# Kernel optimization log

Hardware: AMD Instinct MI355X
Metric: run time of the kernel (lower is better)

Reference implementation:

```python
import jax, jax.numpy as jnp
import numpy as np

R1, R2 = 0.1, 0.2  # initial_radius(0.0125) * 8, * 16
EPS = 1e-5

def sqdist(a, b):
    # a [B,N,3], b [B,M,3] -> [B,N,M]
    return jnp.sum(a * a, -1)[:, :, None] + jnp.sum(b * b, -1)[:, None, :] - 2.0 * jnp.einsum('bnc,bmc->bnm', a, b)

def gather(p, idx):
    # p [B,N,C], idx [B,...] -> [B,...,C]
    return jax.vmap(lambda pp, ii: pp[ii])(p, idx)

def fps(xyz, npoint):
    # farthest point sampling, returns int32 [B,npoint]
    B, N, _ = xyz.shape
    def step(carry, _):
        dist, far = carry
        cen = xyz[jnp.arange(B), far]                       # [B,3]
        d = jnp.sum((xyz - cen[:, None, :]) ** 2, -1)       # [B,N]
        dist = jnp.minimum(dist, d)
        nxt = jnp.argmax(dist, -1).astype(jnp.int32)
        return (dist, nxt), far
    init = (jnp.full((B, N), 1e10, xyz.dtype), jnp.zeros(B, jnp.int32))
    _, idx = jax.lax.scan(step, init, None, length=npoint)
    return idx.T

def ball_query(xyz, new_xyz, radius, nsample):
    d = sqdist(new_xyz, xyz)                                # [B,S,N]
    N = xyz.shape[1]
    cand = jnp.where(d <= radius * radius, jnp.arange(N, dtype=jnp.int32), jnp.int32(N))
    idx = -jax.lax.top_k(-cand, nsample)[0]                 # smallest nsample in-ball indices
    first = idx[..., :1]
    idx = jnp.where(idx == N, first, idx)                   # pad with first neighbor
    nearest = jnp.argmin(d, -1, keepdims=True).astype(jnp.int32)
    return jnp.where(idx == N, nearest, idx)                # fallback if ball empty

def bn_relu(x, g, b, axes):
    # training-mode batchnorm (biased var) + relu, channel-last
    m = jnp.mean(x, axes, keepdims=True)
    v = jnp.mean((x - m) ** 2, axes, keepdims=True)
    return jax.nn.relu((x - m) * jax.lax.rsqrt(v + EPS) * g + b)

def set_abstraction(xyz, feat, npoint, radius, nsample, layers):
    new_xyz = gather(xyz, fps(xyz, npoint))                 # [B,S,3]
    gidx = ball_query(xyz, new_xyz, radius, nsample)        # [B,S,K]
    gx = gather(xyz, gidx) - new_xyz[:, :, None, :]         # [B,S,K,3]
    h = jnp.concatenate([gx, gather(feat, gidx)], -1)       # [B,S,K,3+C]
    for w, g, b in layers:
        h = bn_relu(jnp.einsum('bskc,oc->bsko', h, w), g, b, (0, 1, 2))
    return new_xyz, jnp.max(h, 2)                           # [B,S,Cout]

def set_upconv(pos1, pos2, feat1, feat2, nsample, w1, g1, b1, w2, g2, b2):
    idx = jax.lax.top_k(-sqdist(pos1, pos2), nsample)[1]    # knn into sparse cloud [B,N,K]
    gp = gather(pos2, idx) - pos1[:, :, None, :]
    h = jnp.concatenate([gather(feat2, idx), gp], -1)       # [B,N,K,C2+3]
    h = bn_relu(jnp.einsum('bnkc,oc->bnko', h, w1), g1, b1, (0, 1, 2))
    h = jnp.max(h, 2)
    h = jnp.concatenate([h, feat1], -1)                     # [B,N,mlp[-1]+C1]
    return bn_relu(jnp.einsum('bnc,oc->bno', h, w2), g2, b2, (0, 1))

def feature_prop(pos1, pos2, feat1, feat2, w, g, b):
    negd, idx = jax.lax.top_k(-sqdist(pos1, pos2), 3)       # 3-NN
    dist = jnp.maximum(-negd, 1e-10)
    wgt = 1.0 / dist
    wgt = wgt / jnp.sum(wgt, -1, keepdims=True)
    interp = jnp.sum(gather(feat2, idx) * wgt[..., None], 2)
    h = jnp.concatenate([interp, feat1], -1)
    return bn_relu(jnp.einsum('bnc,oc->bno', h, w), g, b, (0, 1))

def _forward(points1, fea1, points2, fea2,
             sa1_w0, sa1_g0, sa1_b0, sa1_w1, sa1_g1, sa1_b1,
             sa2_w0, sa2_g0, sa2_b0, sa2_w1, sa2_g1, sa2_b1,
             su1_w1, su1_g1, su1_b1, su1_w2, su1_g2, su1_b2,
             fp_w, fp_g, fp_b, bn1_g, bn1_b, conv2_w, conv2_b):
    def pipeline(pts, fea):
        l1x, l1f = set_abstraction(pts, fea, 4096, R1, 16,
                                   [(sa1_w0, sa1_g0, sa1_b0), (sa1_w1, sa1_g1, sa1_b1)])
        l2x, l2f = set_abstraction(l1x, l1f, 1024, R2, 16,
                                   [(sa2_w0, sa2_g0, sa2_b0), (sa2_w1, sa2_g1, sa2_b1)])
        l1n = set_upconv(l1x, l2x, l1f, l2f, 8, su1_w1, su1_g1, su1_b1, su1_w2, su1_g2, su1_b2)
        l0n = feature_prop(pts, l1x, fea, l1n, fp_w, fp_g, fp_b)
        x = bn_relu(l0n, bn1_g, bn1_b, (0, 1))              # relu(bn1(.))
        sf = jnp.einsum('bnc,oc->bno', x, conv2_w) + conv2_b
        return jnp.concatenate([pts, sf], -1)               # include_pos
    return jnp.stack([pipeline(points1, fea1), pipeline(points2, fea2)])  # [2,B,N,19]

def setup_inputs() -> dict:
    key = jax.random.key(0)
    ks = jax.random.split(key, 12)
    B, N, C = 2, 8192, 10
    def w(k, o, i):
        return jax.random.normal(k, (o, i), jnp.float32) * 0.1
    inp = {
        'points1': jax.random.uniform(ks[0], (B, N, 3), jnp.float32),
        'fea1': jax.random.normal(ks[1], (B, N, C), jnp.float32),
        'points2': jax.random.uniform(ks[2], (B, N, 3), jnp.float32),
        'fea2': jax.random.normal(ks[3], (B, N, C), jnp.float32),
        'sa1_w0': w(ks[4], 16, 13), 'sa1_g0': jnp.ones(16), 'sa1_b0': jnp.zeros(16),
        'sa1_w1': w(ks[5], 32, 16), 'sa1_g1': jnp.ones(32), 'sa1_b1': jnp.zeros(32),
        'sa2_w0': w(ks[6], 32, 35), 'sa2_g0': jnp.ones(32), 'sa2_b0': jnp.zeros(32),
        'sa2_w1': w(ks[7], 64, 32), 'sa2_g1': jnp.ones(64), 'sa2_b1': jnp.zeros(64),
        'su1_w1': w(ks[8], 32, 67), 'su1_g1': jnp.ones(32), 'su1_b1': jnp.zeros(32),
        'su1_w2': w(ks[9], 32, 64), 'su1_g2': jnp.ones(32), 'su1_b2': jnp.zeros(32),
        'fp_w': w(ks[10], 32, 42), 'fp_g': jnp.ones(32), 'fp_b': jnp.zeros(32),
        'bn1_g': jnp.ones(32), 'bn1_b': jnp.zeros(32),
        'conv2_w': w(ks[11], 16, 32), 'conv2_b': jnp.zeros(16),
    }
    return inp

def reference(points1, fea1, points2, fea2,
              sa1_w0, sa1_g0, sa1_b0, sa1_w1, sa1_g1, sa1_b1,
              sa2_w0, sa2_g0, sa2_b0, sa2_w1, sa2_g1, sa2_b1,
              su1_w1, su1_g1, su1_b1, su1_w2, su1_g2, su1_b2,
              fp_w, fp_g, fp_b, bn1_g, bn1_b, conv2_w, conv2_b):
    return _forward(points1, fea1, points2, fea2,
                    sa1_w0, sa1_g0, sa1_b0, sa1_w1, sa1_g1, sa1_b1,
                    sa2_w0, sa2_g0, sa2_b0, sa2_w1, sa2_g1, sa2_b1,
                    su1_w1, su1_g1, su1_b1, su1_w2, su1_g2, su1_b2,
                    fp_w, fp_g, fp_b, bn1_g, bn1_b, conv2_w, conv2_b)
```

## Files before the change

### kernel.cpp

```cpp
#include <hip/hip_runtime.h>

#define DI __device__ __forceinline__

enum : int {
  OFF_XYZF = 0,
  OFF_FEAF = OFF_XYZF + 4*8192*3,
  OFF_NX1  = OFF_FEAF + 4*8192*10,
  OFF_L1F  = OFF_NX1  + 4*4096*3,
  OFF_NX2  = OFF_L1F  + 4*4096*32,
  OFF_L2F  = OFF_NX2  + 4*1024*3,
  OFF_UH2  = OFF_L2F  + 4*1024*64,
  OFF_L1N  = OFF_UH2  + 4*4096*32,
  OFF_H3   = OFF_L1N  + 4*4096*32,
  OFF_L0N  = OFF_H3   + 4*8192*32,
  OFF_STATS= OFF_L0N  + 4*8192*32,
  OFF_GIDX1= OFF_STATS + 2048,
  OFF_GIDX2= OFF_GIDX1 + 4*4096*16,
  OFF_UIDX = OFF_GIDX2 + 4*1024*16,
  WS_END   = OFF_UIDX + 4*4096*8
};
enum : int { ST_SA1A=0, ST_SA1B=64, ST_SA2A=128, ST_SA2B=192, ST_U1=320, ST_U2=384, ST_FP=448, ST_BN1=512 };

DI float nrm3(float x, float y, float z){ return fmaf(z,z, fmaf(y,y, x*x)); }
DI float dot3(float ax,float ay,float az,float bx,float by,float bz){
  return fmaf(az,bz, fmaf(ay,by, ax*bx));
}

template<int CTRL>
DI float dppmax_f(float v){
  int o = __builtin_amdgcn_update_dpp(0, __float_as_int(v), CTRL, 0xf, 0xf, true);
  return fmaxf(v, __int_as_float(o));
}
template<int CTRL>
DI int dppmin_i(int v){
  int o = __builtin_amdgcn_update_dpp(0x7fffffff, v, CTRL, 0xf, 0xf, false);
  return v < o ? v : o;
}
DI float red63_fmax(float v){
  v = dppmax_f<0x111>(v);
  v = dppmax_f<0x112>(v);
  v = dppmax_f<0x114>(v);
  v = dppmax_f<0x118>(v);
  v = dppmax_f<0x142>(v);
  v = dppmax_f<0x143>(v);
  return v;
}
DI int red63_imin(int v){
  v = dppmin_i<0x111>(v);
  v = dppmin_i<0x112>(v);
  v = dppmin_i<0x114>(v);
  v = dppmin_i<0x118>(v);
  v = dppmin_i<0x142>(v);
  v = dppmin_i<0x143>(v);
  return v;
}

template<int CH>
DI void stats_accum(float* h, float* dst, float (*sred)[128])
{
  float sq[CH];
  #pragma unroll
  for (int c=0;c<CH;c++) sq[c]=h[c]*h[c];
  #pragma unroll
  for (int m=1;m<64;m<<=1){
    #pragma unroll
    for (int c=0;c<CH;c++){ h[c] += __shfl_xor(h[c], m, 64); sq[c] += __shfl_xor(sq[c], m, 64); }
  }
  const int tid=threadIdx.x, wid=tid>>6, lane=tid&63;
  if (lane==0){
    #pragma unroll
    for (int c=0;c<CH;c++){ sred[wid][c]=h[c]; sred[wid][CH+c]=sq[c]; }
  }
  __syncthreads();
  if (tid < 2*CH){
    float v = sred[0][tid]+sred[1][tid]+sred[2][tid]+sred[3][tid];
    atomicAdd(dst+tid, v);
  }
}

__global__ __launch_bounds__(256) void prep(const float* __restrict__ p1,const float* __restrict__ f1,
                                            const float* __restrict__ p2,const float* __restrict__ f2,
                                            float* __restrict__ xyzf, float* __restrict__ feaf)
{
  const int i = blockIdx.x*256+threadIdx.x;
  const int z = i>>13, n = i&8191, pipe=z>>1, b=z&1;
  const float* ps = (pipe?p2:p1) + (b*8192+n)*3;
  const float* fs = (pipe?f2:f1) + (b*8192+n)*10;
  float* xo = xyzf + (z*8192+n)*3;
  float* fo = feaf + (z*8192+n)*10;
  #pragma unroll
  for (int c=0;c<3;c++)  xo[c]=ps[c];
  #pragma unroll
  for (int c=0;c<10;c++) fo[c]=fs[c];
}

DI int mspread(int v){ return (v&1) | ((v&2)<<2) | ((v&4)<<4); }

template<int N,int NPOINT>
__global__ __launch_bounds__(512) void fps_lane(const float* __restrict__ src, float* __restrict__ dst)
{
  constexpr int T=512, P=N/T;
  const int z = blockIdx.x;
  const float* xyz = src + z*N*3;
  float* nx = dst + z*NPOINT*3;
  const int t = threadIdx.x, w = t>>6, lane = t&63;

  __shared__ float sx[N], sy[N], szz[N];
  __shared__ int hist[512], offs[512], wsum[8];
  __shared__ int sidx[N];
  __shared__ unsigned long long s_wk[2][8];

  hist[t]=0;
  __syncthreads();
  int code_[P];
  #pragma unroll
  for (int i=0;i<P;i++){
    const int j = t + i*T;
    float x=xyz[j*3], y=xyz[j*3+1], zz=xyz[j*3+2];
    sx[j]=x; sy[j]=y; szz[j]=zz;
    int a=(int)(x*8.f);  a=a<0?0:(a>7?7:a);
    int b=(int)(y*8.f);  b=b<0?0:(b>7?7:b);
    int c=(int)(zz*8.f); c=c<0?0:(c>7?7:c);
    int mc = mspread(a) | (mspread(b)<<1) | (mspread(c)<<2);
    code_[i]=mc;
    atomicAdd(&hist[mc],1);
  }
  __syncthreads();
  {
    int x = hist[t];
    int ix = x;
    #pragma unroll
    for (int m=1;m<64;m<<=1){ int y=__shfl_up(ix,m,64); if (lane>=m) ix+=y; }
    if (lane==63) wsum[w]=ix;
    __syncthreads();
    int base=0;
    #pragma unroll
    for (int q=0;q<7;q++) base += (q<w)? wsum[q] : 0;
    offs[t] = base + ix - x;
  }
  __syncthreads();
  #pragma unroll
  for (int i=0;i<P;i++){
    int pos = atomicAdd(&offs[code_[i]],1);
    sidx[pos] = t + i*T;
  }
  __syncthreads();
  float px[P],py[P],pz[P],dist[P]; int oi[P];
  #pragma unroll
  for (int k=0;k<P;k++){
    const int j = sidx[t*P+k];
    oi[k]=j;
    px[k]=sx[j]; py[k]=sy[j]; pz[k]=szz[j];
    dist[k]=1e10f;
  }
  float blox=px[0],bhix=px[0],bloy=py[0],bhiy=py[0],bloz=pz[0],bhiz=pz[0];
  int jb = oi[0];
  #pragma unroll
  for (int k=1;k<P;k++){
    blox=fminf(blox,px[k]); bhix=fmaxf(bhix,px[k]);
    bloy=fminf(bloy,py[k]); bhiy=fmaxf(bhiy,py[k]);
    bloz=fminf(bloz,pz[k]); bhiz=fmaxf(bhiz,pz[k]);
    jb = oi[k]<jb ? oi[k] : jb;
  }
  float lm = 1e10f;

  for (int s=0;;s++){
    float wmv = red63_fmax(lm);
    float swm = __int_as_float(__builtin_amdgcn_readlane(__float_as_int(wmv), 63));
    int jc = (lm==swm) ? jb : 0x7fffffff;
    int jcv = red63_imin(jc);
    int sjw = __builtin_amdgcn_readlane(jcv, 63);
    if (lane==0)
      s_wk[s&1][w] = ((unsigned long long)__float_as_uint(swm)<<32)
                   | (unsigned)(N-1-sjw);
    __syncthreads();
    unsigned long long bk = s_wk[s&1][0];
    #pragma unroll
    for (int q=1;q<8;q++){ unsigned long long o=s_wk[s&1][q]; bk = o>bk?o:bk; }
    const int cur = (N-1) - (int)(unsigned)(bk & 0xffffffffull);
    if (t==0){ nx[s*3]=sx[cur]; nx[s*3+1]=sy[cur]; nx[s*3+2]=szz[cur]; }
    if (s==NPOINT-1) break;
    const float cx=sx[cur], cy=sy[cur], cz=szz[cur];
    float dxm = fmaxf(fmaxf(blox-cx, cx-bhix), 0.f);
    float dym = fmaxf(fmaxf(bloy-cy, cy-bhiy), 0.f);
    float dzm = fmaxf(fmaxf(bloz-cz, cz-bhiz), 0.f);
    float lb  = fmaf(dzm,dzm, fmaf(dym,dym, dxm*dxm));
    if (lb*0.99999f < lm){
      float a=-1.f, b2=-1.f;
      #pragma unroll
      for (int k=0;k<P;k+=2){
        float dx0=px[k]-cx,   dy0=py[k]-cy,   dz0=pz[k]-cz;
        float dx1=px[k+1]-cx, dy1=py[k+1]-cy, dz1=pz[k+1]-cz;
        float d0 = fmaf(dz0,dz0, fmaf(dy0,dy0, dx0*dx0));
        float d1 = fmaf(dz1,dz1, fmaf(dy1,dy1, dx1*dx1));
        float n0 = fminf(dist[k],   d0);
        float n1 = fminf(dist[k+1], d1);
        dist[k]=n0; dist[k+1]=n1;
        a=fmaxf(a,n0); b2=fmaxf(b2,n1);
      }
      lm = fmaxf(a,b2);
      int nj = 0x7fffffff;
      #pragma unroll
      for (int k=0;k<P;k++){
        int cand = (dist[k]==lm) ? oi[k] : 0x7fffffff;
        nj = cand<nj ? cand : nj;
      }
      jb = nj;
    }
  }
}

template<int NSRC,int SQ,int K>
__global__ __launch_bounds__(64) void ball_query(const float* __restrict__ qxyz, const float* __restrict__ sxyz,
                                                 int* __restrict__ gidx, float r2)
{
  __shared__ float4 tile[1024];
  const int z = blockIdx.y, tid = threadIdx.x;
  const int s = blockIdx.x*64 + tid;
  const float* q = qxyz + (z*SQ+s)*3;
  const float qx=q[0],qy=q[1],qz=q[2];
  const float qq=nrm3(qx,qy,qz);
  int cnt=0, first=0, amin=0; float dmin=3.0e38f;
  int* out = gidx + (z*SQ+s)*K;
  for (int t0=0;t0<NSRC;t0+=1024){
    __syncthreads();
    for (int i=tid;i<1024;i+=64){
      const float* p = sxyz + (z*NSRC+t0+i)*3;
      float x=p[0],y=p[1],w=p[2];
      tile[i]=make_float4(x,y,w,nrm3(x,y,w));
    }
    __syncthreads();
    for (int jj=0;jj<1024;jj++){
      float4 p = tile[jj];
      float dot=dot3(qx,qy,qz,p.x,p.y,p.z);
      float d=(qq+p.w)-2.0f*dot;
      const int j = t0+jj;
      if (d < dmin){ dmin=d; amin=j; }
      if (d <= r2 && cnt < K){ if(cnt==0) first=j; out[cnt]=j; cnt++; }
    }
  }
  const int fill = (cnt==0)? amin : first;
  for (int c=cnt;c<K;c++) out[c]=fill;
}

template<int S,int K,int CF,int C1,int C2,int NSRC,int PASS>
__global__ __launch_bounds__(256) void sa_pass(
    const float* __restrict__ srcxyz, const float* __restrict__ srcfea,
    const float* __restrict__ qxyz, const int* __restrict__ gidx,
    const float* __restrict__ w0, const float* __restrict__ g0, const float* __restrict__ b0,
    const float* __restrict__ w1, const float* __restrict__ g1v, const float* __restrict__ b1v,
    float* __restrict__ stats, int offA, int offB, float cnt0, float cnt1,
    float* __restrict__ outp)
{
  constexpr int CIN = 3+CF;
  __shared__ float w0l[C1*CIN];
  __shared__ float w1l[PASS>=2 ? C2*C1 : 1];
  __shared__ float sc0[C1], bi0[C1];
  __shared__ float sc1[C2], bi1[C2];
  __shared__ float sred[4][128];
  const int z = blockIdx.y, pipe = z>>1, tid = threadIdx.x;
  float* stA = stats + pipe*1024 + offA;
  float* stB = stats + pipe*1024 + offB;
  for (int i=tid;i<C1*CIN;i+=256) w0l[i]=w0[i];
  if (PASS>=2){
    for (int i=tid;i<C2*C1;i+=256) w1l[i]=w1[i];
    if (tid<C1){
      float m = stA[tid]/cnt0;
      float var = stA[C1+tid]/cnt0 - m*m;
      float rs = 1.0f/sqrtf(var+1e-5f);
      float sc = rs*g0[tid];
      sc0[tid]=sc; bi0[tid]=b0[tid]-m*sc;
    }
  }
  if (PASS==3 && tid<C2){
    float m = stB[tid]/cnt1;
    float var = stB[C2+tid]/cnt1 - m*m;
    float rs = 1.0f/sqrtf(var+1e-5f);
    float sc = rs*g1v[tid];
    sc1[tid]=sc; bi1[tid]=b1v[tid]-m*sc;
  }
  __syncthreads();
  const int item = blockIdx.x*256+tid;
  const int s = item/K;
  const int j = gidx[(z*S+s)*K + (item%K)];
  const float* q = qxyz + (z*S+s)*3;
  const float* p = srcxyz + (z*NSRC+j)*3;
  float f[CIN];
  f[0]=p[0]-q[0]; f[1]=p[1]-q[1]; f[2]=p[2]-q[2];
  const float* fe = srcfea + (z*NSRC+j)*CF;
  #pragma unroll
  for (int c=0;c<CF;c++) f[3+c]=fe[c];
  float h1[C1];
  #pragma unroll
  for (int o=0;o<C1;o++){
    float a=0.f;
    #pragma unroll
    for (int c=0;c<CIN;c++) a = fmaf(w0l[o*CIN+c], f[c], a);
    h1[o]=a;
  }
  if (PASS==1){ stats_accum<C1>(h1, stA, sred); return; }
  float f2v[C1];
  #pragma unroll
  for (int o=0;o<C1;o++) f2v[o]=fmaxf(fmaf(h1[o],sc0[o],bi0[o]), 0.f);
  float h2[C2];
  #pragma unroll
  for (int o=0;o<C2;o++){
    float a=0.f;
    #pragma unroll
    for (int c=0;c<C1;c++) a = fmaf(w1l[o*C1+c], f2v[c], a);
    h2[o]=a;
  }
  if (PASS==2){ stats_accum<C2>(h2, stB, sred); return; }
  #pragma unroll
  for (int o=0;o<C2;o++) h2[o]=fmaxf(fmaf(h2[o],sc1[o],bi1[o]), 0.f);
  #pragma unroll
  for (int msk=1; msk<K; msk<<=1){
    #pragma unroll
    for (int o=0;o<C2;o++) h2[o]=fmaxf(h2[o], __shfl_xor(h2[o], msk, 64));
  }
  if ((tid & (K-1))==0){
    float* op = outp + (z*S+s)*C2;
    #pragma unroll
    for (int o=0;o<C2;o++) op[o]=h2[o];
  }
}

__global__ __launch_bounds__(64) void up_top8(const float* __restrict__ nx1, const float* __restrict__ nx2,
                                              int* __restrict__ uidx)
{
  __shared__ float4 tile[1024];
  const int z=blockIdx.y, tid=threadIdx.x;
  const int s=blockIdx.x*64+tid;
  const float* q = nx1 + (z*4096+s)*3;
  const float qx=q[0],qy=q[1],qz=q[2];
  const float qq=nrm3(qx,qy,qz);
  for (int i=tid;i<1024;i+=64){
    const float* p = nx2 + (z*1024+i)*3;
    float x=p[0],y=p[1],w=p[2];
    tile[i]=make_float4(x,y,w,nrm3(x,y,w));
  }
  __syncthreads();
  float d[8]; int id[8];
  #pragma unroll
  for (int r=0;r<8;r++){ d[r]=3e38f; id[r]=0; }
  for (int j=0;j<1024;j++){
    float4 p=tile[j];
    float dt=dot3(qx,qy,qz,p.x,p.y,p.z);
    float dd=(qq+p.w)-2.0f*dt;
    if (dd<d[7]){
      d[7]=dd; id[7]=j;
      #pragma unroll
      for (int r=7;r>0;r--){
        if (d[r]<d[r-1]){ float td=d[r-1]; d[r-1]=d[r]; d[r]=td; int ti=id[r-1]; id[r-1]=id[r]; id[r]=ti; }
      }
    }
  }
  int* o = uidx + (z*4096+s)*8;
  #pragma unroll
  for (int r=0;r<8;r++) o[r]=id[r];
}

template<int PASS>
__global__ __launch_bounds__(256) void up_pass(
    const float* __restrict__ nx1, const float* __restrict__ nx2,
    const float* __restrict__ l2f, const float* __restrict__ l1f,
    const int* __restrict__ uidx,
    const float* __restrict__ w1, const float* __restrict__ g1v, const float* __restrict__ b1v,
    const float* __restrict__ w2,
    float* __restrict__ stats, float* __restrict__ uh2)
{
  __shared__ float w1l[32*67];
  __shared__ float w2l[PASS==2?32*64:1];
  __shared__ float sc0[32], bi0[32];
  __shared__ float sred[4][128];
  const int z=blockIdx.y, pipe=z>>1, tid=threadIdx.x;
  float* stU1 = stats + pipe*1024 + ST_U1;
  float* stU2 = stats + pipe*1024 + ST_U2;
  for (int i=tid;i<32*67;i+=256) w1l[i]=w1[i];
  if (PASS==2){
    for (int i=tid;i<32*64;i+=256) w2l[i]=w2[i];
    if (tid<32){
      float m=stU1[tid]/65536.f;
      float var=stU1[32+tid]/65536.f - m*m;
      float rs=1.0f/sqrtf(var+1e-5f);
      float sc=rs*g1v[tid];
      sc0[tid]=sc; bi0[tid]=b1v[tid]-m*sc;
    }
  }
  __syncthreads();
  const int item = blockIdx.x*256+tid;
  const int s = item>>3, k = item&7;
  const int j = uidx[(z*4096+s)*8+k];
  float f67[67];
  const float* fe = l2f + (z*1024+j)*64;
  #pragma unroll
  for (int c=0;c<64;c++) f67[c]=fe[c];
  const float* pp = nx2 + (z*1024+j)*3;
  const float* qv = nx1 + (z*4096+s)*3;
  f67[64]=pp[0]-qv[0]; f67[65]=pp[1]-qv[1]; f67[66]=pp[2]-qv[2];
  float h[32];
  #pragma unroll
  for (int o=0;o<32;o++){
    float a=0.f;
    #pragma unroll
    for (int c=0;c<67;c++) a=fmaf(w1l[o*67+c], f67[c], a);
    h[o]=a;
  }
  if (PASS==1){ stats_accum<32>(h, stU1, sred); return; }
  #pragma unroll
  for (int o=0;o<32;o++) h[o]=fmaxf(fmaf(h[o],sc0[o],bi0[o]),0.f);
  #pragma unroll
  for (int msk=1; msk<8; msk<<=1){
    #pragma unroll
    for (int o=0;o<32;o++) h[o]=fmaxf(h[o], __shfl_xor(h[o],msk,64));
  }
  float h2[32];
  if (k==0){
    const float* l1 = l1f + (z*4096+s)*32;
    #pragma unroll
    for (int o=0;o<32;o++){
      float a=0.f;
      #pragma unroll
      for (int c=0;c<32;c++) a=fmaf(w2l[o*64+c], h[c], a);
      #pragma unroll
      for (int c=0;c<32;c++) a=fmaf(w2l[o*64+32+c], l1[c], a);
      h2[o]=a;
    }
    float* up = uh2 + (z*4096+s)*32;
    #pragma unroll
    for (int o=0;o<32;o++) up[o]=h2[o];
  } else {
    #pragma unroll
    for (int o=0;o<32;o++) h2[o]=0.f;
  }
  stats_accum<32>(h2, stU2, sred);
}

__global__ __launch_bounds__(256) void up_norm(const float* __restrict__ uh2, const float* __restrict__ g,
                                               const float* __restrict__ b, const float* __restrict__ stats,
                                               float* __restrict__ l1n)
{
  const int i = blockIdx.x*256+threadIdx.x;
  const int z = i>>17, pipe = z>>1, c = i&31;
  const float* st = stats + pipe*1024 + ST_U2;
  float m = st[c]/8192.f;
  float var = st[32+c]/8192.f - m*m;
  float rs = 1.0f/sqrtf(var+1e-5f);
  float sc = rs*g[c];
  float bi = b[c]-m*sc;
  l1n[i]=fmaxf(fmaf(uh2[i],sc,bi),0.f);
}

__global__ __launch_bounds__(256) void fp_kern(
  const float* __restrict__ xyzf, const float* __restrict__ feaf,
  const float* __restrict__ nx1, const float* __restrict__ l1n,
  const float* __restrict__ fpw, float* __restrict__ stats, float* __restrict__ h3)
{
  __shared__ float4 tile[2048];
  __shared__ float wl[32*42];
  __shared__ float sred[4][128];
  const int z=blockIdx.y, pipe=z>>1, tid=threadIdx.x;
  for (int i=tid;i<32*42;i+=256) wl[i]=fpw[i];
  const int n = blockIdx.x*256+tid;
  const float* q = xyzf + (z*8192+n)*3;
  const float qx=q[0],qy=q[1],qz=q[2];
  const float qq2=nrm3(qx,qy,qz);
  float d0=3e38f,d1=3e38f,d2=3e38f; int i0=0,i1=0,i2=0;
  for (int t0=0;t0<4096;t0+=2048){
    __syncthreads();
    for (int i=tid;i<2048;i+=256){
      const float* p = nx1 + (z*4096+t0+i)*3;
      float x=p[0],y=p[1],w=p[2];
      tile[i]=make_float4(x,y,w,nrm3(x,y,w));
    }
    __syncthreads();
    for (int jj=0;jj<2048;jj++){
      float4 p=tile[jj];
      float dt=dot3(qx,qy,qz,p.x,p.y,p.z);
      float d=(qq2+p.w)-2.0f*dt;
      if (d<d2){
        d2=d; i2=t0+jj;
        if (d2<d1){ float td=d1; d1=d2; d2=td; int ti=i1; i1=i2; i2=ti; }
        if (d1<d0){ float td=d0; d0=d1; d1=td; int ti=i0; i0=i1; i1=ti; }
      }
    }
  }
  d0=fmaxf(d0,1e-10f); d1=fmaxf(d1,1e-10f); d2=fmaxf(d2,1e-10f);
  float w0=1.0f/d0, w1=1.0f/d1, w2=1.0f/d2;
  float wsum=(w0+w1)+w2;
  w0/=wsum; w1/=wsum; w2/=wsum;
  const float* A = l1n + (z*4096+i0)*32;
  const float* B = l1n + (z*4096+i1)*32;
  const float* C = l1n + (z*4096+i2)*32;
  float f[42];
  #pragma unroll
  for (int c=0;c<32;c++) f[c]=fmaf(C[c],w2, fmaf(B[c],w1, A[c]*w0));
  const float* fe = feaf + (z*8192+n)*10;
  #pragma unroll
  for (int c=0;c<10;c++) f[32+c]=fe[c];
  float h[32];
  #pragma unroll
  for (int o=0;o<32;o++){
    float a=0.f;
    #pragma unroll
    for (int c=0;c<42;c++) a=fmaf(wl[o*42+c], f[c], a);
    h[o]=a;
    h3[(z*8192+n)*32+o]=a;
  }
  stats_accum<32>(h, stats + pipe*1024 + ST_FP, sred);
}

__global__ __launch_bounds__(256) void fp_post(const float* __restrict__ h3, const float* __restrict__ g,
                                               const float* __restrict__ b, float* __restrict__ stats,
                                               float* __restrict__ l0n)
{
  __shared__ float sc[32], bi[32];
  __shared__ float sred[4][128];
  const int tid=threadIdx.x;
  const int row = blockIdx.x*256+tid;
  const int pipe = row>>14;
  float* stF = stats + pipe*1024 + ST_FP;
  float* stB = stats + pipe*1024 + ST_BN1;
  if (tid<32){
    float m=stF[tid]/16384.f;
    float var=stF[32+tid]/16384.f-m*m;
    float rs=1.0f/sqrtf(var+1e-5f);
    float s=rs*g[tid];
    sc[tid]=s; bi[tid]=b[tid]-m*s;
  }
  __syncthreads();
  float x[32];
  #pragma unroll
  for (int c=0;c<32;c++){ x[c]=fmaxf(fmaf(h3[row*32+c],sc[c],bi[c]),0.f); l0n[row*32+c]=x[c]; }
  stats_accum<32>(x, stB, sred);
}

__global__ __launch_bounds__(256) void final_kern(
  const float* __restrict__ l0n, const float* __restrict__ g, const float* __restrict__ b,
  const float* __restrict__ cw, const float* __restrict__ cb,
  const float* __restrict__ p1, const float* __restrict__ p2,
  const float* __restrict__ stats, float* __restrict__ out)
{
  __shared__ float sc[32], bi[32], wl[512], bl[16];
  const int tid=threadIdx.x;
  const int row = blockIdx.x*256+tid;
  const int z=row>>13, pipe=z>>1, bb=z&1, n=row&8191;
  const float* st = stats + pipe*1024 + ST_BN1;
  if (tid<32){
    float m=st[tid]/16384.f;
    float var=st[32+tid]/16384.f-m*m;
    float rs=1.0f/sqrtf(var+1e-5f);
    float s=rs*g[tid];
    sc[tid]=s; bi[tid]=b[tid]-m*s;
  }
  for (int i=tid;i<512;i+=256) wl[i]=cw[i];
  if (tid<16) bl[tid]=cb[tid];
  __syncthreads();
  float x[32];
  #pragma unroll
  for (int c=0;c<32;c++) x[c]=fmaxf(fmaf(l0n[row*32+c],sc[c],bi[c]),0.f);
  float* o = out + row*19;
  const float* ps = (pipe?p2:p1) + (bb*8192+n)*3;
  o[0]=ps[0]; o[1]=ps[1]; o[2]=ps[2];
  #pragma unroll
  for (int oo=0;oo<16;oo++){
    float a=0.f;
    #pragma unroll
    for (int c=0;c<32;c++) a=fmaf(wl[oo*32+c],x[c],a);
    o[3+oo]=a+bl[oo];
  }
}

extern "C" void kernel_launch(void* const* d_in, const int* in_sizes, int n_in,
                              void* d_out, int out_size, void* d_ws, size_t ws_size,
                              hipStream_t stream)
{
  (void)in_sizes; (void)n_in; (void)out_size; (void)ws_size;
  const float* p1 = (const float*)d_in[0];
  const float* f1 = (const float*)d_in[1];
  const float* p2 = (const float*)d_in[2];
  const float* f2 = (const float*)d_in[3];
  const float *sa1_w0=(const float*)d_in[4], *sa1_g0=(const float*)d_in[5], *sa1_b0=(const float*)d_in[6];
  const float *sa1_w1=(const float*)d_in[7], *sa1_g1=(const float*)d_in[8], *sa1_b1=(const float*)d_in[9];
  const float *sa2_w0=(const float*)d_in[10],*sa2_g0=(const float*)d_in[11],*sa2_b0=(const float*)d_in[12];
  const float *sa2_w1=(const float*)d_in[13],*sa2_g1=(const float*)d_in[14],*sa2_b1=(const float*)d_in[15];
  const float *su1_w1=(const float*)d_in[16],*su1_g1=(const float*)d_in[17],*su1_b1=(const float*)d_in[18];
  const float *su1_w2=(const float*)d_in[19],*su1_g2=(const float*)d_in[20],*su1_b2=(const float*)d_in[21];
  const float *fp_w=(const float*)d_in[22], *fp_g=(const float*)d_in[23], *fp_b=(const float*)d_in[24];
  const float *bn1_g=(const float*)d_in[25],*bn1_b=(const float*)d_in[26];
  const float *conv2_w=(const float*)d_in[27],*conv2_b=(const float*)d_in[28];
  float* wsf=(float*)d_ws; int* wsi=(int*)d_ws;
  float* xyzf=wsf+OFF_XYZF; float* feaf=wsf+OFF_FEAF;
  float* nx1=wsf+OFF_NX1; float* l1f=wsf+OFF_L1F;
  float* nx2=wsf+OFF_NX2; float* l2f=wsf+OFF_L2F;
  float* uh2=wsf+OFF_UH2; float* l1n=wsf+OFF_L1N;
  float* h3=wsf+OFF_H3; float* l0n=wsf+OFF_L0N;
  float* stats=wsf+OFF_STATS;
  int* gidx1=wsi+OFF_GIDX1; int* gidx2=wsi+OFF_GIDX2; int* uidx=wsi+OFF_UIDX;
  const float R2A=(float)(0.1*0.1), R2B=(float)(0.2*0.2);

  (void)hipMemsetAsync(stats, 0, 2048*sizeof(float), stream);
  prep<<<128,256,0,stream>>>(p1,f1,p2,f2,xyzf,feaf);
  fps_lane<8192,4096><<<4,512,0,stream>>>(xyzf, nx1);
  ball_query<8192,4096,16><<<dim3(64,4),64,0,stream>>>(nx1, xyzf, gidx1, R2A);
  sa_pass<4096,16,10,16,32,8192,1><<<dim3(256,4),256,0,stream>>>(xyzf,feaf,nx1,gidx1,
      sa1_w0,sa1_g0,sa1_b0,sa1_w1,sa1_g1,sa1_b1, stats,ST_SA1A,ST_SA1B,131072.f,131072.f, l1f);
  sa_pass<4096,16,10,16,32,8192,2><<<dim3(256,4),256,0,stream>>>(xyzf,feaf,nx1,gidx1,
      sa1_w0,sa1_g0,sa1_b0,sa1_w1,sa1_g1,sa1_b1, stats,ST_SA1A,ST_SA1B,131072.f,131072.f, l1f);
  sa_pass<4096,16,10,16,32,8192,3><<<dim3(256,4),256,0,stream>>>(xyzf,feaf,nx1,gidx1,
      sa1_w0,sa1_g0,sa1_b0,sa1_w1,sa1_g1,sa1_b1, stats,ST_SA1A,ST_SA1B,131072.f,131072.f, l1f);
  fps_lane<4096,1024><<<4,512,0,stream>>>(nx1, nx2);
  ball_query<4096,1024,16><<<dim3(16,4),64,0,stream>>>(nx2, nx1, gidx2, R2B);
  sa_pass<1024,16,32,32,64,4096,1><<<dim3(64,4),256,0,stream>>>(nx1,l1f,nx2,gidx2,
      sa2_w0,sa2_g0,sa2_b0,sa2_w1,sa2_g1,sa2_b1, stats,ST_SA2A,ST_SA2B,32768.f,32768.f, l2f);
  sa_pass<1024,16,32,32,64,4096,2><<<dim3(64,4),256,0,stream>>>(nx1,l1f,nx2,gidx2,
      sa2_w0,sa2_g0,sa2_b0,sa2_w1,sa2_g1,sa2_b1, stats,ST_SA2A,ST_SA2B,32768.f,32768.f, l2f);
  sa_pass<1024,16,32,32,64,4096,3><<<dim3(64,4),256,0,stream>>>(nx1,l1f,nx2,gidx2,
      sa2_w0,sa2_g0,sa2_b0,sa2_w1,sa2_g1,sa2_b1, stats,ST_SA2A,ST_SA2B,32768.f,32768.f, l2f);
  up_top8<<<dim3(64,4),64,0,stream>>>(nx1,nx2,uidx);
  up_pass<1><<<dim3(128,4),256,0,stream>>>(nx1,nx2,l2f,l1f,uidx,su1_w1,su1_g1,su1_b1,su1_w2,stats,uh2);
  up_pass<2><<<dim3(128,4),256,0,stream>>>(nx1,nx2,l2f,l1f,uidx,su1_w1,su1_g1,su1_b1,su1_w2,stats,uh2);
  up_norm<<<2048,256,0,stream>>>(uh2,su1_g2,su1_b2,stats,l1n);
  fp_kern<<<dim3(32,4),256,0,stream>>>(xyzf,feaf,nx1,l1n,fp_w,stats,h3);
  fp_post<<<128,256,0,stream>>>(h3,fp_g,fp_b,stats,l0n);
  final_kern<<<128,256,0,stream>>>(l0n,bn1_g,bn1_b,conv2_w,conv2_b,p1,p2,stats,(float*)d_out);
}
```

Measured before the change: 6.792 ms.

## Pack FPS distance and index into one double key, carry winner coordinates

```diff
diff --git a/kernel.cpp b/kernel.cpp
--- a/kernel.cpp
+++ b/kernel.cpp
@@ -27,32 +27,30 @@
 }
 
 template<int CTRL>
-DI float dppmax_f(float v){
-  int o = __builtin_amdgcn_update_dpp(0, __float_as_int(v), CTRL, 0xf, 0xf, true);
-  return fmaxf(v, __int_as_float(o));
-}
-template<int CTRL>
-DI int dppmin_i(int v){
-  int o = __builtin_amdgcn_update_dpp(0x7fffffff, v, CTRL, 0xf, 0xf, false);
-  return v < o ? v : o;
-}
-DI float red63_fmax(float v){
-  v = dppmax_f<0x111>(v);
-  v = dppmax_f<0x112>(v);
-  v = dppmax_f<0x114>(v);
-  v = dppmax_f<0x118>(v);
-  v = dppmax_f<0x142>(v);
-  v = dppmax_f<0x143>(v);
+DI double kstage(double v){
+  int lo = __builtin_amdgcn_update_dpp(0, __double2loint(v), CTRL, 0xf, 0xf, true);
+  int hi = __builtin_amdgcn_update_dpp(0, __double2hiint(v), CTRL, 0xf, 0xf, true);
+  return fmax(v, __hiloint2double(hi, lo));
+}
+DI double red63_kmax(double v){
+  v = kstage<0x111>(v);
+  v = kstage<0x112>(v);
+  v = kstage<0x114>(v);
+  v = kstage<0x118>(v);
+  v = kstage<0x142>(v);
+  v = kstage<0x143>(v);
   return v;
 }
-DI int red63_imin(int v){
-  v = dppmin_i<0x111>(v);
-  v = dppmin_i<0x112>(v);
-  v = dppmin_i<0x114>(v);
-  v = dppmin_i<0x118>(v);
-  v = dppmin_i<0x142>(v);
-  v = dppmin_i<0x143>(v);
-  return v;
+
+struct Ent { double k; float x,y,z; };
+DI Ent emax(Ent a, Ent b){
+  bool c = b.k > a.k;
+  Ent r;
+  r.k = c ? b.k : a.k;
+  r.x = c ? b.x : a.x;
+  r.y = c ? b.y : a.y;
+  r.z = c ? b.z : a.z;
+  return r;
 }
 
 template<int CH>
@@ -97,7 +95,7 @@
 DI int mspread(int v){ return (v&1) | ((v&2)<<2) | ((v&4)<<4); }
 
 template<int N,int NPOINT>
-__global__ __launch_bounds__(512) void fps_lane(const float* __restrict__ src, float* __restrict__ dst)
+__global__ __launch_bounds__(512) void fps_wave(const float* __restrict__ src, float* __restrict__ dst)
 {
   constexpr int T=512, P=N/T;
   const int z = blockIdx.x;
@@ -108,7 +106,9 @@
   __shared__ float sx[N], sy[N], szz[N];
   __shared__ int hist[512], offs[512], wsum[8];
   __shared__ int sidx[N];
-  __shared__ unsigned long long s_wk[2][8];
+  __shared__ int swin[NPOINT];
+  __shared__ double s_wk[2][8];
+  __shared__ float4 s_wc[2][8];
 
   hist[t]=0;
   __syncthreads();
@@ -155,32 +155,41 @@
   }
   float blox=px[0],bhix=px[0],bloy=py[0],bhiy=py[0],bloz=pz[0],bhiz=pz[0];
   int jb = oi[0];
+  float bx=px[0], by=py[0], bz=pz[0];
   #pragma unroll
   for (int k=1;k<P;k++){
     blox=fminf(blox,px[k]); bhix=fmaxf(bhix,px[k]);
     bloy=fminf(bloy,py[k]); bhiy=fmaxf(bhiy,py[k]);
     bloz=fminf(bloz,pz[k]); bhiz=fmaxf(bhiz,pz[k]);
-    jb = oi[k]<jb ? oi[k] : jb;
+    bool c = oi[k]<jb;
+    jb = c?oi[k]:jb; bx = c?px[k]:bx; by = c?py[k]:by; bz = c?pz[k]:bz;
   }
   float lm = 1e10f;
+  double mykey = __hiloint2double(__float_as_int(1e10f), N-1-jb);
 
   for (int s=0;;s++){
-    float wmv = red63_fmax(lm);
-    float swm = __int_as_float(__builtin_amdgcn_readlane(__float_as_int(wmv), 63));
-    int jc = (lm==swm) ? jb : 0x7fffffff;
-    int jcv = red63_imin(jc);
-    int sjw = __builtin_amdgcn_readlane(jcv, 63);
-    if (lane==0)
-      s_wk[s&1][w] = ((unsigned long long)__float_as_uint(swm)<<32)
-                   | (unsigned)(N-1-sjw);
+    const int buf = s&1;
+    double wk = red63_kmax(mykey);
+    int glo = __builtin_amdgcn_readlane(__double2loint(wk), 63);
+    int ghi = __builtin_amdgcn_readlane(__double2hiint(wk), 63);
+    double skey = __hiloint2double(ghi, glo);
+    if (mykey == skey){
+      s_wk[buf][w] = mykey;
+      s_wc[buf][w] = make_float4(bx,by,bz,0.f);
+    }
     __syncthreads();
-    unsigned long long bk = s_wk[s&1][0];
-    #pragma unroll
-    for (int q=1;q<8;q++){ unsigned long long o=s_wk[s&1][q]; bk = o>bk?o:bk; }
-    const int cur = (N-1) - (int)(unsigned)(bk & 0xffffffffull);
-    if (t==0){ nx[s*3]=sx[cur]; nx[s*3+1]=sy[cur]; nx[s*3+2]=szz[cur]; }
+    Ent e[8];
+    #pragma unroll
+    for (int q=0;q<8;q++){
+      e[q].k = s_wk[buf][q];
+      float4 c = s_wc[buf][q];
+      e[q].x=c.x; e[q].y=c.y; e[q].z=c.z;
+    }
+    Ent g = emax(emax(emax(e[0],e[1]),emax(e[2],e[3])),
+                 emax(emax(e[4],e[5]),emax(e[6],e[7])));
+    if (t==0) swin[s] = (N-1) - __double2loint(g.k);
     if (s==NPOINT-1) break;
-    const float cx=sx[cur], cy=sy[cur], cz=szz[cur];
+    const float cx=g.x, cy=g.y, cz=g.z;
     float dxm = fmaxf(fmaxf(blox-cx, cx-bhix), 0.f);
     float dym = fmaxf(fmaxf(bloy-cy, cy-bhiy), 0.f);
     float dzm = fmaxf(fmaxf(bloz-cz, cz-bhiz), 0.f);
@@ -199,14 +208,20 @@
         a=fmaxf(a,n0); b2=fmaxf(b2,n1);
       }
       lm = fmaxf(a,b2);
-      int nj = 0x7fffffff;
+      int nj = 0x7fffffff; float nbx=0.f,nby=0.f,nbz=0.f;
       #pragma unroll
       for (int k=0;k<P;k++){
-        int cand = (dist[k]==lm) ? oi[k] : 0x7fffffff;
-        nj = cand<nj ? cand : nj;
+        bool c = (dist[k]==lm) && (oi[k]<nj);
+        nj = c?oi[k]:nj; nbx = c?px[k]:nbx; nby = c?py[k]:nby; nbz = c?pz[k]:nbz;
       }
-      jb = nj;
-    }
+      jb=nj; bx=nbx; by=nby; bz=nbz;
+      mykey = __hiloint2double(__float_as_int(lm), N-1-jb);
+    }
+  }
+  __syncthreads();
+  for (int i=t;i<NPOINT;i+=T){
+    int j = swin[i];
+    nx[i*3]=sx[j]; nx[i*3+1]=sy[j]; nx[i*3+2]=szz[j];
   }
 }
 
@@ -601,7 +616,7 @@
 
   (void)hipMemsetAsync(stats, 0, 2048*sizeof(float), stream);
   prep<<<128,256,0,stream>>>(p1,f1,p2,f2,xyzf,feaf);
-  fps_lane<8192,4096><<<4,512,0,stream>>>(xyzf, nx1);
+  fps_wave<8192,4096><<<4,512,0,stream>>>(xyzf, nx1);
   ball_query<8192,4096,16><<<dim3(64,4),64,0,stream>>>(nx1, xyzf, gidx1, R2A);
   sa_pass<4096,16,10,16,32,8192,1><<<dim3(256,4),256,0,stream>>>(xyzf,feaf,nx1,gidx1,
       sa1_w0,sa1_g0,sa1_b0,sa1_w1,sa1_g1,sa1_b1, stats,ST_SA1A,ST_SA1B,131072.f,131072.f, l1f);
@@ -609,7 +624,7 @@
       sa1_w0,sa1_g0,sa1_b0,sa1_w1,sa1_g1,sa1_b1, stats,ST_SA1A,ST_SA1B,131072.f,131072.f, l1f);
   sa_pass<4096,16,10,16,32,8192,3><<<dim3(256,4),256,0,stream>>>(xyzf,feaf,nx1,gidx1,
       sa1_w0,sa1_g0,sa1_b0,sa1_w1,sa1_g1,sa1_b1, stats,ST_SA1A,ST_SA1B,131072.f,131072.f, l1f);
-  fps_lane<4096,1024><<<4,512,0,stream>>>(nx1, nx2);
+  fps_wave<4096,1024><<<4,512,0,stream>>>(nx1, nx2);
   ball_query<4096,1024,16><<<dim3(16,4),64,0,stream>>>(nx2, nx1, gidx2, R2B);
   sa_pass<1024,16,32,32,64,4096,1><<<dim3(64,4),256,0,stream>>>(nx1,l1f,nx2,gidx2,
       sa2_w0,sa2_g0,sa2_b0,sa2_w1,sa2_g1,sa2_b1, stats,ST_SA2A,ST_SA2B,32768.f,32768.f, l2f);
```

Result: slower. 8.093 ms (+19.2%).
